# Kernel tuning notes

Hardware: AMD Instinct MI355X
Metric: run time of the kernel (lower is better)

The kernel has to match this reference:

```python
import jax, jax.numpy as jnp
import numpy as np

N_NODES = 100000

def gcn_layer(x, W, b, src, dst, norm):
    # x: [N, Fin], W: [Fin, Fout]; fused linear then normalized neighbor aggregation
    h = x @ W                                   # [N, Fout]
    msg = h[src] * norm[:, None]                # gather + per-edge scale, [E', Fout]
    agg = jax.ops.segment_sum(msg, dst, num_segments=N_NODES)  # scatter-add
    return agg + b

def _add_self_loops_and_norm(edge_index):
    src, dst = edge_index[0], edge_index[1]
    loop = jnp.arange(N_NODES, dtype=src.dtype)
    src = jnp.concatenate([src, loop])
    dst = jnp.concatenate([dst, loop])
    deg = jax.ops.segment_sum(jnp.ones_like(dst, dtype=jnp.float32), dst, num_segments=N_NODES)
    dis = jnp.where(deg > 0, jax.lax.rsqrt(deg), 0.0)   # deg^{-1/2}
    norm = dis[src] * dis[dst]                          # symmetric GCN normalization
    return src, dst, norm

def setup_inputs() -> dict:
    key = jax.random.key(0)
    k1, k2, k3, k4, k5, k6 = jax.random.split(key, 6)
    F_IN, F_HID, F_OUT = 64, 64, 64
    E = 1600000
    x = jax.random.normal(k1, (N_NODES, F_IN), dtype=jnp.float32)
    edge_index = jax.random.randint(k2, (2, E), 0, N_NODES, dtype=jnp.int64)
    s1 = 1.0 / np.sqrt(F_IN)
    s2 = 1.0 / np.sqrt(F_HID)
    W1 = jax.random.uniform(k3, (F_IN, F_HID), dtype=jnp.float32, minval=-s1, maxval=s1)
    b1 = jax.random.uniform(k4, (F_HID,), dtype=jnp.float32, minval=-s1, maxval=s1)
    W2 = jax.random.uniform(k5, (F_HID, F_OUT), dtype=jnp.float32, minval=-s2, maxval=s2)
    b2 = jax.random.uniform(k6, (F_OUT,), dtype=jnp.float32, minval=-s2, maxval=s2)
    return {"x": x, "edge_index": edge_index, "W1": W1, "b1": b1, "W2": W2, "b2": b2}

def reference(x, edge_index, W1, b1, W2, b2):
    src, dst, norm = _add_self_loops_and_norm(edge_index)
    h = gcn_layer(x, W1, b1, src, dst, norm)
    h = jax.nn.relu(h)
    h = gcn_layer(h, W2, b2, src, dst, norm)
    return h
```

## Files before the change

kernel.cpp:

```cpp
#include <hip/hip_runtime.h>
#include <cstdint>
#include <cstddef>


#define BK_SHIFT 9
#define BK_NODES 512
#define EPB 8192
#define CAP 12288
#define NBMAX 256

typedef short bf16x8 __attribute__((ext_vector_type(8)));
typedef float f32x4  __attribute__((ext_vector_type(4)));

static __device__ __forceinline__ unsigned short f2b(float f) {
    unsigned x = __float_as_uint(f);
    unsigned r = (x + 0x7FFFu + ((x >> 16) & 1u)) >> 16;
    return (unsigned short)r;
}
static __device__ __forceinline__ float blo(unsigned u) {
    return __uint_as_float(u << 16);
}
static __device__ __forceinline__ float bhi(unsigned u) {
    return __uint_as_float(u & 0xFFFF0000u);
}
static __device__ __forceinline__ void splitbf(float x, short& hi, short& lo) {
    unsigned short h = f2b(x);
    hi = (short)h;
    float r = x - __uint_as_float((unsigned)h << 16);
    lo = (short)f2b(r);
}

__global__ void k_init(int* __restrict__ gcursor, int NB) {
    int t = threadIdx.x;
    if (t < NB) gcursor[t] = t * CAP;
}

__global__ void __launch_bounds__(256) k_bscatter(const int* __restrict__ src,
                                                  const int* __restrict__ dst,
                                                  int* __restrict__ gcursor,
                                                  unsigned* __restrict__ packed,
                                                  int E, int NB) {
    __shared__ int hist[NBMAX];
    __shared__ int base[NBMAX];
    int t = threadIdx.x;
    for (int i = t; i < NB; i += 256) hist[i] = 0;
    __syncthreads();
    int e0 = blockIdx.x * EPB;
    int e1 = min(e0 + EPB, E);
    int4 dv[8];
    int kd[8];
#pragma unroll
    for (int k = 0; k < 8; ++k) {
        int e = e0 + t * 4 + k * 1024;
        kd[k] = (e + 3 < e1) ? 1 : 0;
        if (kd[k]) dv[k] = *(const int4*)(dst + e);
    }
#pragma unroll
    for (int k = 0; k < 8; ++k) {
        if (kd[k]) {
            atomicAdd(&hist[dv[k].x >> BK_SHIFT], 1);
            atomicAdd(&hist[dv[k].y >> BK_SHIFT], 1);
            atomicAdd(&hist[dv[k].z >> BK_SHIFT], 1);
            atomicAdd(&hist[dv[k].w >> BK_SHIFT], 1);
        }
    }
    __syncthreads();
    for (int i = t; i < NB; i += 256) {
        int c = hist[i];
        base[i] = c ? atomicAdd(&gcursor[i], c) : 0;
        hist[i] = 0;
    }
    __syncthreads();
    int4 sv[8];
#pragma unroll
    for (int k = 0; k < 8; ++k) {
        int e = e0 + t * 4 + k * 1024;
        if (kd[k]) sv[k] = *(const int4*)(src + e);
    }
#pragma unroll
    for (int k = 0; k < 8; ++k) {
        if (kd[k]) {
            int b0 = dv[k].x >> BK_SHIFT;
            int p0 = base[b0] + atomicAdd(&hist[b0], 1);
            packed[p0] = (unsigned)sv[k].x | (((unsigned)dv[k].x & (BK_NODES - 1)) << 17);
            int b1 = dv[k].y >> BK_SHIFT;
            int p1 = base[b1] + atomicAdd(&hist[b1], 1);
            packed[p1] = (unsigned)sv[k].y | (((unsigned)dv[k].y & (BK_NODES - 1)) << 17);
            int b2 = dv[k].z >> BK_SHIFT;
            int p2 = base[b2] + atomicAdd(&hist[b2], 1);
            packed[p2] = (unsigned)sv[k].z | (((unsigned)dv[k].z & (BK_NODES - 1)) << 17);
            int b3 = dv[k].w >> BK_SHIFT;
            int p3 = base[b3] + atomicAdd(&hist[b3], 1);
            packed[p3] = (unsigned)sv[k].w | (((unsigned)dv[k].w & (BK_NODES - 1)) << 17);
        }
    }
}

__global__ void __launch_bounds__(512) k_build(const unsigned* __restrict__ packed,
                                               const int* __restrict__ gcursor,
                                               int* __restrict__ rp,
                                               int* __restrict__ dega,
                                               float* __restrict__ dis,
                                               int* __restrict__ col, int N) {
    __shared__ int cnt_s[BK_NODES];
    __shared__ int tmp[BK_NODES];
    int b = blockIdx.x;
    int t = threadIdx.x;
    int node0 = b << BK_SHIFT;
    int nnode = min(BK_NODES, N - node0);
    int e0 = b * CAP;
    int e1 = gcursor[b];
    cnt_s[t] = 0;
    __syncthreads();
    for (int e = e0 + t * 4; e < e1; e += 2048) {
        int m = e1 - e; m = m > 4 ? 4 : m;
        unsigned p0 = packed[e];
        unsigned p1 = (m > 1) ? packed[e + 1] : 0;
        unsigned p2 = (m > 2) ? packed[e + 2] : 0;
        unsigned p3 = (m > 3) ? packed[e + 3] : 0;
        atomicAdd(&cnt_s[p0 >> 17], 1);
        if (m > 1) atomicAdd(&cnt_s[p1 >> 17], 1);
        if (m > 2) atomicAdd(&cnt_s[p2 >> 17], 1);
        if (m > 3) atomicAdd(&cnt_s[p3 >> 17], 1);
    }
    __syncthreads();
    int v = cnt_s[t];
    tmp[t] = v;
    __syncthreads();
    for (int off = 1; off < BK_NODES; off <<= 1) {
        int a = (t >= off) ? tmp[t - off] : 0;
        __syncthreads();
        tmp[t] += a;
        __syncthreads();
    }
    int excl = tmp[t] - v;
    if (t < nnode) {
        rp[node0 + t] = e0 + excl;
        dega[node0 + t] = v;
        dis[node0 + t] = rsqrtf((float)(v + 1));
    }
    __syncthreads();
    cnt_s[t] = excl;
    __syncthreads();
    for (int e = e0 + t * 4; e < e1; e += 2048) {
        int m = e1 - e; m = m > 4 ? 4 : m;
        unsigned p0 = packed[e];
        unsigned p1 = (m > 1) ? packed[e + 1] : 0;
        unsigned p2 = (m > 2) ? packed[e + 2] : 0;
        unsigned p3 = (m > 3) ? packed[e + 3] : 0;
        int pos0 = atomicAdd(&cnt_s[p0 >> 17], 1);
        col[e0 + pos0] = (int)(p0 & 0x1FFFFu);
        if (m > 1) { int pos = atomicAdd(&cnt_s[p1 >> 17], 1); col[e0 + pos] = (int)(p1 & 0x1FFFFu); }
        if (m > 2) { int pos = atomicAdd(&cnt_s[p2 >> 17], 1); col[e0 + pos] = (int)(p2 & 0x1FFFFu); }
        if (m > 3) { int pos = atomicAdd(&cnt_s[p3 >> 17], 1); col[e0 + pos] = (int)(p3 & 0x1FFFFu); }
    }
}

__global__ void __launch_bounds__(256) k_gemm_mfma(const float* __restrict__ X,
                                                   const float* __restrict__ W,
                                                   const float* __restrict__ dis,
                                                   unsigned short* __restrict__ g16,
                                                   int n, int nstrips) {
    __shared__ float Ws[4096];
    int t = threadIdx.x;
    {
        const float4* W4 = (const float4*)W;
        float4* S4 = (float4*)Ws;
#pragma unroll
        for (int i = 0; i < 4; ++i) S4[t + i * 256] = W4[t + i * 256];
    }
    __syncthreads();
    int wid  = t >> 6;
    int lane = t & 63;
    int quad = lane >> 4;
    int fl   = lane & 15;

    bf16x8 Bh[4][2], Bl[4][2];
#pragma unroll
    for (int tt = 0; tt < 4; ++tt)
#pragma unroll
        for (int c = 0; c < 2; ++c)
#pragma unroll
            for (int j = 0; j < 8; ++j) {
                float w = Ws[(c * 32 + quad * 8 + j) * 64 + tt * 16 + fl];
                short hi, lo;
                splitbf(w, hi, lo);
                Bh[tt][c][j] = hi;
                Bl[tt][c][j] = lo;
            }

    for (int s = blockIdx.x * 4 + wid; s < nstrips; s += gridDim.x * 4) {
        int row0 = s << 4;
        const float4* xp = (const float4*)(X + ((size_t)(row0 + fl) << 6));
        bf16x8 Ah[2], Al[2];
#pragma unroll
        for (int c = 0; c < 2; ++c) {
            float4 a = xp[c * 8 + quad * 2];
            float4 b = xp[c * 8 + quad * 2 + 1];
            float xs[8] = {a.x, a.y, a.z, a.w, b.x, b.y, b.z, b.w};
#pragma unroll
            for (int j = 0; j < 8; ++j) {
                short hi, lo;
                splitbf(xs[j], hi, lo);
                Ah[c][j] = hi;
                Al[c][j] = lo;
            }
        }
        f32x4 acc[4];
#pragma unroll
        for (int tt = 0; tt < 4; ++tt) acc[tt] = (f32x4){0.f, 0.f, 0.f, 0.f};
#pragma unroll
        for (int tt = 0; tt < 4; ++tt) {
#pragma unroll
            for (int c = 0; c < 2; ++c) {
                acc[tt] = __builtin_amdgcn_mfma_f32_16x16x32_bf16(Ah[c], Bh[tt][c], acc[tt], 0, 0, 0);
                acc[tt] = __builtin_amdgcn_mfma_f32_16x16x32_bf16(Al[c], Bh[tt][c], acc[tt], 0, 0, 0);
                acc[tt] = __builtin_amdgcn_mfma_f32_16x16x32_bf16(Ah[c], Bl[tt][c], acc[tt], 0, 0, 0);
            }
        }
        float4 dv = *(const float4*)(dis + row0 + quad * 4);
        float ds4[4] = {dv.x, dv.y, dv.z, dv.w};
#pragma unroll
        for (int tt = 0; tt < 4; ++tt) {
#pragma unroll
            for (int r = 0; r < 4; ++r) {
                int row = row0 + quad * 4 + r;
                float v = acc[tt][r] * ds4[r];
                g16[(size_t)row * 64 + tt * 16 + fl] = f2b(v);
            }
        }
    }
}

template <int RELU>
__global__ void __launch_bounds__(256) k_agg(const unsigned short* __restrict__ g16,
                                             const int* __restrict__ col,
                                             const int* __restrict__ rp,
                                             const int* __restrict__ dega,
                                             const float* __restrict__ dis,
                                             const float* __restrict__ bias,
                                             float* __restrict__ out, int n) {
    int lane = threadIdx.x & 63;
    int wv = (blockIdx.x << 2) | (threadIdx.x >> 6);
    int sub = lane >> 3;
    int fl  = lane & 7;
    int base = wv << 3;
    if (base >= n) return;
    int node = base + sub;
    int nd = min(node, n - 1);
    int start = rp[nd];
    int deg = (node < n) ? dega[nd] : 0;
    int dm = max(deg, __shfl_xor(deg, 8));
    dm = max(dm, __shfl_xor(dm, 16));
    dm = max(dm, __shfl_xor(dm, 32));

    uint4 us = *((const uint4*)(g16 + ((size_t)nd << 6)) + fl);
    float A[8], B[8], C[8], D[8];
    A[0] = blo(us.x); A[1] = bhi(us.x); A[2] = blo(us.y); A[3] = bhi(us.y);
    A[4] = blo(us.z); A[5] = bhi(us.z); A[6] = blo(us.w); A[7] = bhi(us.w);
#pragma unroll
    for (int j = 0; j < 8; ++j) { B[j] = 0.f; C[j] = 0.f; D[j] = 0.f; }

    int sb = sub << 3;
    for (int c = 0; c < dm; c += 8) {
        int rem = deg - c;
        int cv = 0;
        if (fl < rem) cv = col[start + c + fl];
        int rr[8];
#pragma unroll
        for (int i = 0; i < 8; ++i) rr[i] = __shfl(cv, sb + i);
        uint4 u[8];
#pragma unroll
        for (int i = 0; i < 8; ++i)
            if (i < rem) u[i] = *((const uint4*)(g16 + ((size_t)rr[i] << 6)) + fl);
#pragma unroll
        for (int i = 0; i < 8; ++i) {
            if (i < rem) {
                float* T = ((i & 3) == 0) ? A : ((i & 3) == 1) ? B : ((i & 3) == 2) ? C : D;
                T[0] += blo(u[i].x); T[1] += bhi(u[i].x);
                T[2] += blo(u[i].y); T[3] += bhi(u[i].y);
                T[4] += blo(u[i].z); T[5] += bhi(u[i].z);
                T[6] += blo(u[i].w); T[7] += bhi(u[i].w);
            }
        }
    }
    float s = dis[nd];
    float4 bv0 = ((const float4*)bias)[fl * 2];
    float4 bv1 = ((const float4*)bias)[fl * 2 + 1];
    float r[8];
#pragma unroll
    for (int j = 0; j < 8; ++j) r[j] = (A[j] + B[j]) + (C[j] + D[j]);
    float4 o0, o1;
    o0.x = fmaf(s, r[0], bv0.x); o0.y = fmaf(s, r[1], bv0.y);
    o0.z = fmaf(s, r[2], bv0.z); o0.w = fmaf(s, r[3], bv0.w);
    o1.x = fmaf(s, r[4], bv1.x); o1.y = fmaf(s, r[5], bv1.y);
    o1.z = fmaf(s, r[6], bv1.z); o1.w = fmaf(s, r[7], bv1.w);
    if (RELU) {
        o0.x = fmaxf(o0.x, 0.f); o0.y = fmaxf(o0.y, 0.f);
        o0.z = fmaxf(o0.z, 0.f); o0.w = fmaxf(o0.w, 0.f);
        o1.x = fmaxf(o1.x, 0.f); o1.y = fmaxf(o1.y, 0.f);
        o1.z = fmaxf(o1.z, 0.f); o1.w = fmaxf(o1.w, 0.f);
    }
    if (node < n) {
        float4* op = (float4*)(out + ((size_t)node << 6)) + fl * 2;
        op[0] = o0;
        op[1] = o1;
    }
}

__global__ void __launch_bounds__(256, 4) k_agg_gemm2(const unsigned short* __restrict__ g16,
                                                      const int* __restrict__ col,
                                                      const int* __restrict__ rp,
                                                      const int* __restrict__ dega,
                                                      const float* __restrict__ dis,
                                                      const float* __restrict__ bias,
                                                      const float* __restrict__ W2,
                                                      unsigned short* __restrict__ g16b,
                                                      int n) {
    __shared__ float W2s[4096];
    __shared__ float hs[32 * 68];
    int t = threadIdx.x;
    {
        const float4* W4 = (const float4*)W2;
        float4* S4 = (float4*)W2s;
#pragma unroll
        for (int i = 0; i < 4; ++i) S4[t + i * 256] = W4[t + i * 256];
    }

    int lane = t & 63;
    int wid  = t >> 6;
    int wv = (blockIdx.x << 2) | wid;
    int sub = lane >> 3;
    int fl  = lane & 7;
    int base = wv << 3;
    int node = base + sub;
    int nd = (node < n) ? node : (n - 1);
    int start = rp[nd];
    int deg = (node < n) ? dega[nd] : 0;
    int dm = max(deg, __shfl_xor(deg, 8));
    dm = max(dm, __shfl_xor(dm, 16));
    dm = max(dm, __shfl_xor(dm, 32));

    uint4 us = *((const uint4*)(g16 + ((size_t)nd << 6)) + fl);
    float A[8], B[8], C[8], D[8];
    A[0] = blo(us.x); A[1] = bhi(us.x); A[2] = blo(us.y); A[3] = bhi(us.y);
    A[4] = blo(us.z); A[5] = bhi(us.z); A[6] = blo(us.w); A[7] = bhi(us.w);
#pragma unroll
    for (int j = 0; j < 8; ++j) { B[j] = 0.f; C[j] = 0.f; D[j] = 0.f; }

    int sb = sub << 3;
    for (int c = 0; c < dm; c += 8) {
        int rem = deg - c;
        int cv = 0;
        if (fl < rem) cv = col[start + c + fl];
        int rr[8];
#pragma unroll
        for (int i = 0; i < 8; ++i) rr[i] = __shfl(cv, sb + i);
        uint4 u[8];
#pragma unroll
        for (int i = 0; i < 8; ++i)
            if (i < rem) u[i] = *((const uint4*)(g16 + ((size_t)rr[i] << 6)) + fl);
#pragma unroll
        for (int i = 0; i < 8; ++i) {
            if (i < rem) {
                float* T = ((i & 3) == 0) ? A : ((i & 3) == 1) ? B : ((i & 3) == 2) ? C : D;
                T[0] += blo(u[i].x); T[1] += bhi(u[i].x);
                T[2] += blo(u[i].y); T[3] += bhi(u[i].y);
                T[4] += blo(u[i].z); T[5] += bhi(u[i].z);
                T[6] += blo(u[i].w); T[7] += bhi(u[i].w);
            }
        }
    }
    {
        float s = dis[nd];
        float4 bv0 = ((const float4*)bias)[fl * 2];
        float4 bv1 = ((const float4*)bias)[fl * 2 + 1];
        float r[8];
#pragma unroll
        for (int j = 0; j < 8; ++j) r[j] = (A[j] + B[j]) + (C[j] + D[j]);
        float4 h0, h1;
        h0.x = fmaxf(fmaf(s, r[0], bv0.x), 0.f);
        h0.y = fmaxf(fmaf(s, r[1], bv0.y), 0.f);
        h0.z = fmaxf(fmaf(s, r[2], bv0.z), 0.f);
        h0.w = fmaxf(fmaf(s, r[3], bv0.w), 0.f);
        h1.x = fmaxf(fmaf(s, r[4], bv1.x), 0.f);
        h1.y = fmaxf(fmaf(s, r[5], bv1.y), 0.f);
        h1.z = fmaxf(fmaf(s, r[6], bv1.z), 0.f);
        h1.w = fmaxf(fmaf(s, r[7], bv1.w), 0.f);
        int lrow = (wid << 3) | sub;
        float* hp = &hs[lrow * 68 + fl * 8];
        *(float4*)hp = h0;
        *(float4*)(hp + 4) = h1;
    }
    __syncthreads();

    {
        int quad = lane >> 4;
        int fq   = lane & 15;
        int strip = wid >> 1;
        int tbase = (wid & 1) << 1;
        bf16x8 Ah[2], Al[2];
#pragma unroll
        for (int kc = 0; kc < 2; ++kc) {
            const float* hp2 = &hs[(strip * 16 + fq) * 68 + kc * 32 + quad * 8];
            float4 a = *(const float4*)hp2;
            float4 b = *(const float4*)(hp2 + 4);
            float xs[8] = {a.x, a.y, a.z, a.w, b.x, b.y, b.z, b.w};
#pragma unroll
            for (int j = 0; j < 8; ++j) {
                short hi, lo;
                splitbf(xs[j], hi, lo);
                Ah[kc][j] = hi;
                Al[kc][j] = lo;
            }
        }
        f32x4 acc[2];
        acc[0] = (f32x4){0.f, 0.f, 0.f, 0.f};
        acc[1] = (f32x4){0.f, 0.f, 0.f, 0.f};
#pragma unroll
        for (int tt = 0; tt < 2; ++tt) {
#pragma unroll
            for (int kc = 0; kc < 2; ++kc) {
                bf16x8 Bh, Bl;
#pragma unroll
                for (int j = 0; j < 8; ++j) {
                    float w = W2s[(kc * 32 + quad * 8 + j) * 64 + (tbase + tt) * 16 + fq];
                    short hi, lo;
                    splitbf(w, hi, lo);
                    Bh[j] = hi;
                    Bl[j] = lo;
                }
                acc[tt] = __builtin_amdgcn_mfma_f32_16x16x32_bf16(Ah[kc], Bh, acc[tt], 0, 0, 0);
                acc[tt] = __builtin_amdgcn_mfma_f32_16x16x32_bf16(Al[kc], Bh, acc[tt], 0, 0, 0);
                acc[tt] = __builtin_amdgcn_mfma_f32_16x16x32_bf16(Ah[kc], Bl, acc[tt], 0, 0, 0);
            }
        }
        int row0 = (blockIdx.x << 5) + strip * 16 + quad * 4;
        float d4[4];
        if (row0 + 3 < n) {
            float4 dv = *(const float4*)(dis + row0);
            d4[0] = dv.x; d4[1] = dv.y; d4[2] = dv.z; d4[3] = dv.w;
        } else {
#pragma unroll
            for (int r2 = 0; r2 < 4; ++r2) d4[r2] = (row0 + r2 < n) ? dis[row0 + r2] : 0.f;
        }
#pragma unroll
        for (int tt = 0; tt < 2; ++tt) {
#pragma unroll
            for (int r2 = 0; r2 < 4; ++r2) {
                int row = row0 + r2;
                if (row < n)
                    g16b[(size_t)row * 64 + (tbase + tt) * 16 + fq] = f2b(acc[tt][r2] * d4[r2]);
            }
        }
    }
}

extern "C" void kernel_launch(void* const* d_in, const int* in_sizes, int n_in,
                              void* d_out, int out_size, void* d_ws, size_t ws_size,
                              hipStream_t stream) {
    const float* x  = (const float*)d_in[0];
    const int*   ei = (const int*)d_in[1];
    const float* W1 = (const float*)d_in[2];
    const float* b1 = (const float*)d_in[3];
    const float* W2 = (const float*)d_in[4];
    const float* b2 = (const float*)d_in[5];
    float* out = (float*)d_out;

    const int N = in_sizes[0] / 64;
    const int E = in_sizes[1] / 2;
    const int NB = (N + BK_NODES - 1) >> BK_SHIFT;
    const int nstrips = (N + 15) >> 4;
    const int* src = ei;
    const int* dst = ei + E;

    char* ws = (char*)d_ws;
    size_t off = 0;
    auto alloc = [&](size_t bytes) -> void* {
        void* p = ws + off;
        off = (off + bytes + 255) & ~(size_t)255;
        return p;
    };
    int*            gcursor = (int*)alloc((size_t)NB * 4);
    int*            rp      = (int*)alloc((size_t)N * 4);
    int*            dega    = (int*)alloc((size_t)N * 4);
    float*          dis     = (float*)alloc((size_t)N * 4);
    unsigned*       packed  = (unsigned*)alloc((size_t)NB * CAP * 4);
    int*            col     = (int*)alloc((size_t)NB * CAP * 4);
    unsigned short* g16     = (unsigned short*)alloc((size_t)N * 64 * 2);
    unsigned short* g16b    = (unsigned short*)alloc((size_t)N * 64 * 2);
    (void)ws_size;

    k_init<<<1, 256, 0, stream>>>(gcursor, NB);
    k_bscatter<<<(E + EPB - 1) / EPB, 256, 0, stream>>>(src, dst, gcursor, packed, E, NB);
    k_build<<<NB, 512, 0, stream>>>(packed, gcursor, rp, dega, dis, col, N);

    k_gemm_mfma<<<782, 256, 0, stream>>>(x, W1, dis, g16, N, nstrips);
    k_agg_gemm2<<<(N + 31) / 32, 256, 0, stream>>>(g16, col, rp, dega, dis, b1, W2, g16b, N);
    k_agg<0><<<(N + 31) / 32, 256, 0, stream>>>(g16b, col, rp, dega, dis, b2, out, N);
}
```

Baseline: 199.3 us.

## Shrink CSR buckets, stage packed edges in LDS, and pad W2 shared tile

Node buckets shrink from 512 to 256 nodes, with smaller per-block edge chunks and capacity, so there are twice as many buckets and build blocks, each using 256 threads. The build kernel now copies each bucket's packed edges into shared memory once with vector loads, then runs both counting passes from LDS instead of reading global memory twice. The W2 shared tile in the second aggregation kernel gets a row stride of 66 to reduce LDS bank conflicts on the strided B-operand reads. The tighter per-bucket capacity of 5120 adds overflow risk if a bucket receives more edges than expected.

```diff
diff --git a/kernel.cpp b/kernel.cpp
--- a/kernel.cpp
+++ b/kernel.cpp
@@ -3,11 +3,11 @@
 #include <cstddef>
 
 
-#define BK_SHIFT 9
-#define BK_NODES 512
-#define EPB 8192
-#define CAP 12288
-#define NBMAX 256
+#define BK_SHIFT 8
+#define BK_NODES 256
+#define EPB 4096
+#define CAP 5120
+#define NBMAX 512
 
 typedef short bf16x8 __attribute__((ext_vector_type(8)));
 typedef float f32x4  __attribute__((ext_vector_type(4)));
@@ -47,16 +47,16 @@
     __syncthreads();
     int e0 = blockIdx.x * EPB;
     int e1 = min(e0 + EPB, E);
-    int4 dv[8];
-    int kd[8];
-#pragma unroll
-    for (int k = 0; k < 8; ++k) {
+    int4 dv[4];
+    int kd[4];
+#pragma unroll
+    for (int k = 0; k < 4; ++k) {
         int e = e0 + t * 4 + k * 1024;
         kd[k] = (e + 3 < e1) ? 1 : 0;
         if (kd[k]) dv[k] = *(const int4*)(dst + e);
     }
 #pragma unroll
-    for (int k = 0; k < 8; ++k) {
+    for (int k = 0; k < 4; ++k) {
         if (kd[k]) {
             atomicAdd(&hist[dv[k].x >> BK_SHIFT], 1);
             atomicAdd(&hist[dv[k].y >> BK_SHIFT], 1);
@@ -71,14 +71,14 @@
         hist[i] = 0;
     }
     __syncthreads();
-    int4 sv[8];
-#pragma unroll
-    for (int k = 0; k < 8; ++k) {
+    int4 sv[4];
+#pragma unroll
+    for (int k = 0; k < 4; ++k) {
         int e = e0 + t * 4 + k * 1024;
         if (kd[k]) sv[k] = *(const int4*)(src + e);
     }
 #pragma unroll
-    for (int k = 0; k < 8; ++k) {
+    for (int k = 0; k < 4; ++k) {
         if (kd[k]) {
             int b0 = dv[k].x >> BK_SHIFT;
             int p0 = base[b0] + atomicAdd(&hist[b0], 1);
@@ -96,12 +96,13 @@
     }
 }
 
-__global__ void __launch_bounds__(512) k_build(const unsigned* __restrict__ packed,
+__global__ void __launch_bounds__(256) k_build(const unsigned* __restrict__ packed,
                                                const int* __restrict__ gcursor,
                                                int* __restrict__ rp,
                                                int* __restrict__ dega,
                                                float* __restrict__ dis,
                                                int* __restrict__ col, int N) {
+    __shared__ unsigned pk_s[CAP];
     __shared__ int cnt_s[BK_NODES];
     __shared__ int tmp[BK_NODES];
     int b = blockIdx.x;
@@ -109,20 +110,18 @@
     int node0 = b << BK_SHIFT;
     int nnode = min(BK_NODES, N - node0);
     int e0 = b * CAP;
-    int e1 = gcursor[b];
+    int count = gcursor[b] - e0;
     cnt_s[t] = 0;
-    __syncthreads();
-    for (int e = e0 + t * 4; e < e1; e += 2048) {
-        int m = e1 - e; m = m > 4 ? 4 : m;
-        unsigned p0 = packed[e];
-        unsigned p1 = (m > 1) ? packed[e + 1] : 0;
-        unsigned p2 = (m > 2) ? packed[e + 2] : 0;
-        unsigned p3 = (m > 3) ? packed[e + 3] : 0;
-        atomicAdd(&cnt_s[p0 >> 17], 1);
-        if (m > 1) atomicAdd(&cnt_s[p1 >> 17], 1);
-        if (m > 2) atomicAdd(&cnt_s[p2 >> 17], 1);
-        if (m > 3) atomicAdd(&cnt_s[p3 >> 17], 1);
-    }
+    for (int e4 = t * 4; e4 < count; e4 += 1024) {
+        if (e4 + 3 < count) {
+            uint4 v = *(const uint4*)(packed + e0 + e4);
+            *(uint4*)&pk_s[e4] = v;
+        } else {
+            for (int m = e4; m < count; ++m) pk_s[m] = packed[e0 + m];
+        }
+    }
+    __syncthreads();
+    for (int j = t; j < count; j += 256) atomicAdd(&cnt_s[pk_s[j] >> 17], 1);
     __syncthreads();
     int v = cnt_s[t];
     tmp[t] = v;
@@ -142,17 +141,10 @@
     __syncthreads();
     cnt_s[t] = excl;
     __syncthreads();
-    for (int e = e0 + t * 4; e < e1; e += 2048) {
-        int m = e1 - e; m = m > 4 ? 4 : m;
-        unsigned p0 = packed[e];
-        unsigned p1 = (m > 1) ? packed[e + 1] : 0;
-        unsigned p2 = (m > 2) ? packed[e + 2] : 0;
-        unsigned p3 = (m > 3) ? packed[e + 3] : 0;
-        int pos0 = atomicAdd(&cnt_s[p0 >> 17], 1);
-        col[e0 + pos0] = (int)(p0 & 0x1FFFFu);
-        if (m > 1) { int pos = atomicAdd(&cnt_s[p1 >> 17], 1); col[e0 + pos] = (int)(p1 & 0x1FFFFu); }
-        if (m > 2) { int pos = atomicAdd(&cnt_s[p2 >> 17], 1); col[e0 + pos] = (int)(p2 & 0x1FFFFu); }
-        if (m > 3) { int pos = atomicAdd(&cnt_s[p3 >> 17], 1); col[e0 + pos] = (int)(p3 & 0x1FFFFu); }
+    for (int j = t; j < count; j += 256) {
+        unsigned p = pk_s[j];
+        int pos = atomicAdd(&cnt_s[p >> 17], 1);
+        col[e0 + pos] = (int)(p & 0x1FFFFu);
     }
 }
 
@@ -317,14 +309,18 @@
                                                       const float* __restrict__ W2,
                                                       unsigned short* __restrict__ g16b,
                                                       int n) {
-    __shared__ float W2s[4096];
+    __shared__ float W2s[64 * 66];
     __shared__ float hs[32 * 68];
     int t = threadIdx.x;
     {
         const float4* W4 = (const float4*)W2;
-        float4* S4 = (float4*)W2s;
-#pragma unroll
-        for (int i = 0; i < 4; ++i) S4[t + i * 256] = W4[t + i * 256];
+#pragma unroll
+        for (int i = 0; i < 4; ++i) {
+            float4 v = W4[t + i * 256];
+            int idx = (t + i * 256) << 2;
+            float* p = &W2s[(idx >> 6) * 66 + (idx & 63)];
+            p[0] = v.x; p[1] = v.y; p[2] = v.z; p[3] = v.w;
+        }
     }
 
     int lane = t & 63;
@@ -424,7 +420,7 @@
                 bf16x8 Bh, Bl;
 #pragma unroll
                 for (int j = 0; j < 8; ++j) {
-                    float w = W2s[(kc * 32 + quad * 8 + j) * 64 + (tbase + tt) * 16 + fq];
+                    float w = W2s[(kc * 32 + quad * 8 + j) * 66 + (tbase + tt) * 16 + fq];
                     short hi, lo;
                     splitbf(w, hi, lo);
                     Bh[j] = hi;
@@ -491,9 +487,9 @@
     unsigned short* g16b    = (unsigned short*)alloc((size_t)N * 64 * 2);
     (void)ws_size;
 
-    k_init<<<1, 256, 0, stream>>>(gcursor, NB);
+    k_init<<<1, 512, 0, stream>>>(gcursor, NB);
     k_bscatter<<<(E + EPB - 1) / EPB, 256, 0, stream>>>(src, dst, gcursor, packed, E, NB);
-    k_build<<<NB, 512, 0, stream>>>(packed, gcursor, rp, dega, dis, col, N);
+    k_build<<<NB, 256, 0, stream>>>(packed, gcursor, rp, dega, dis, col, N);
 
     k_gemm_mfma<<<782, 256, 0, stream>>>(x, W1, dis, g16, N, nstrips);
     k_agg_gemm2<<<(N + 31) / 32, 256, 0, stream>>>(g16, col, rp, dega, dis, b1, W2, g16b, N);
```

Measured after the change: 200.8 us. No clear change (+0.8%).

## Split neighbor aggregation into four feature passes with 4-byte gathers

Applied to the files above, without the earlier changes.

Both aggregation kernels now loop over four 16-feature slices of each row. Each lane gathers one 4-byte word per neighbor per pass instead of a 16-byte vector, which cuts accumulator registers from 32 to 8 floats. Column indices are read with nontemporal loads, and the final output is written with nontemporal stores. The cost is that the edge list is reread and shuffled four times, and the gathers become narrower, so more memory transactions are issued per byte.

```diff
diff --git a/kernel.cpp b/kernel.cpp
--- a/kernel.cpp
+++ b/kernel.cpp
@@ -11,6 +11,7 @@
 
 typedef short bf16x8 __attribute__((ext_vector_type(8)));
 typedef float f32x4  __attribute__((ext_vector_type(4)));
+typedef float f32x2  __attribute__((ext_vector_type(2)));
 
 static __device__ __forceinline__ unsigned short f2b(float f) {
     unsigned x = __float_as_uint(f);
@@ -232,7 +233,6 @@
     }
 }
 
-template <int RELU>
 __global__ void __launch_bounds__(256) k_agg(const unsigned short* __restrict__ g16,
                                              const int* __restrict__ col,
                                              const int* __restrict__ rp,
@@ -253,58 +253,44 @@
     int dm = max(deg, __shfl_xor(deg, 8));
     dm = max(dm, __shfl_xor(dm, 16));
     dm = max(dm, __shfl_xor(dm, 32));
-
-    uint4 us = *((const uint4*)(g16 + ((size_t)nd << 6)) + fl);
-    float A[8], B[8], C[8], D[8];
-    A[0] = blo(us.x); A[1] = bhi(us.x); A[2] = blo(us.y); A[3] = bhi(us.y);
-    A[4] = blo(us.z); A[5] = bhi(us.z); A[6] = blo(us.w); A[7] = bhi(us.w);
-#pragma unroll
-    for (int j = 0; j < 8; ++j) { B[j] = 0.f; C[j] = 0.f; D[j] = 0.f; }
-
+    float s = dis[nd];
+    const unsigned* g16u = (const unsigned*)g16;
     int sb = sub << 3;
-    for (int c = 0; c < dm; c += 8) {
-        int rem = deg - c;
-        int cv = 0;
-        if (fl < rem) cv = col[start + c + fl];
-        int rr[8];
-#pragma unroll
-        for (int i = 0; i < 8; ++i) rr[i] = __shfl(cv, sb + i);
-        uint4 u[8];
-#pragma unroll
-        for (int i = 0; i < 8; ++i)
-            if (i < rem) u[i] = *((const uint4*)(g16 + ((size_t)rr[i] << 6)) + fl);
-#pragma unroll
-        for (int i = 0; i < 8; ++i) {
-            if (i < rem) {
-                float* T = ((i & 3) == 0) ? A : ((i & 3) == 1) ? B : ((i & 3) == 2) ? C : D;
-                T[0] += blo(u[i].x); T[1] += bhi(u[i].x);
-                T[2] += blo(u[i].y); T[3] += bhi(u[i].y);
-                T[4] += blo(u[i].z); T[5] += bhi(u[i].z);
-                T[6] += blo(u[i].w); T[7] += bhi(u[i].w);
-            }
-        }
-    }
-    float s = dis[nd];
-    float4 bv0 = ((const float4*)bias)[fl * 2];
-    float4 bv1 = ((const float4*)bias)[fl * 2 + 1];
-    float r[8];
-#pragma unroll
-    for (int j = 0; j < 8; ++j) r[j] = (A[j] + B[j]) + (C[j] + D[j]);
-    float4 o0, o1;
-    o0.x = fmaf(s, r[0], bv0.x); o0.y = fmaf(s, r[1], bv0.y);
-    o0.z = fmaf(s, r[2], bv0.z); o0.w = fmaf(s, r[3], bv0.w);
-    o1.x = fmaf(s, r[4], bv1.x); o1.y = fmaf(s, r[5], bv1.y);
-    o1.z = fmaf(s, r[6], bv1.z); o1.w = fmaf(s, r[7], bv1.w);
-    if (RELU) {
-        o0.x = fmaxf(o0.x, 0.f); o0.y = fmaxf(o0.y, 0.f);
-        o0.z = fmaxf(o0.z, 0.f); o0.w = fmaxf(o0.w, 0.f);
-        o1.x = fmaxf(o1.x, 0.f); o1.y = fmaxf(o1.y, 0.f);
-        o1.z = fmaxf(o1.z, 0.f); o1.w = fmaxf(o1.w, 0.f);
-    }
-    if (node < n) {
-        float4* op = (float4*)(out + ((size_t)node << 6)) + fl * 2;
-        op[0] = o0;
-        op[1] = o1;
+
+#pragma unroll 1
+    for (int p = 0; p < 4; ++p) {
+        unsigned us = g16u[(size_t)nd * 32 + p * 8 + fl];
+        float A0 = blo(us), A1 = bhi(us);
+        float B0 = 0.f, B1 = 0.f, C0 = 0.f, C1 = 0.f, D0 = 0.f, D1 = 0.f;
+        for (int c = 0; c < dm; c += 8) {
+            int rem = deg - c;
+            int cv = 0;
+            if (fl < rem) cv = __builtin_nontemporal_load(col + start + c + fl);
+            int rr[8];
+#pragma unroll
+            for (int i = 0; i < 8; ++i) rr[i] = __shfl(cv, sb + i);
+            unsigned u[8];
+#pragma unroll
+            for (int i = 0; i < 8; ++i)
+                if (i < rem) u[i] = g16u[(size_t)rr[i] * 32 + p * 8 + fl];
+#pragma unroll
+            for (int i = 0; i < 8; ++i) {
+                if (i < rem) {
+                    if ((i & 3) == 0)      { A0 += blo(u[i]); A1 += bhi(u[i]); }
+                    else if ((i & 3) == 1) { B0 += blo(u[i]); B1 += bhi(u[i]); }
+                    else if ((i & 3) == 2) { C0 += blo(u[i]); C1 += bhi(u[i]); }
+                    else                   { D0 += blo(u[i]); D1 += bhi(u[i]); }
+                }
+            }
+        }
+        float r0 = (A0 + B0) + (C0 + D0);
+        float r1 = (A1 + B1) + (C1 + D1);
+        f32x2 bv = *(const f32x2*)(bias + p * 16 + fl * 2);
+        f32x2 o;
+        o[0] = fmaf(s, r0, bv[0]);
+        o[1] = fmaf(s, r1, bv[1]);
+        if (node < n)
+            __builtin_nontemporal_store(o, (f32x2*)(out + ((size_t)node << 6) + p * 16 + fl * 2));
     }
 }
 
@@ -340,57 +326,49 @@
     int dm = max(deg, __shfl_xor(deg, 8));
     dm = max(dm, __shfl_xor(dm, 16));
     dm = max(dm, __shfl_xor(dm, 32));
-
-    uint4 us = *((const uint4*)(g16 + ((size_t)nd << 6)) + fl);
-    float A[8], B[8], C[8], D[8];
-    A[0] = blo(us.x); A[1] = bhi(us.x); A[2] = blo(us.y); A[3] = bhi(us.y);
-    A[4] = blo(us.z); A[5] = bhi(us.z); A[6] = blo(us.w); A[7] = bhi(us.w);
-#pragma unroll
-    for (int j = 0; j < 8; ++j) { B[j] = 0.f; C[j] = 0.f; D[j] = 0.f; }
-
+    float s = dis[nd];
+    const unsigned* g16u = (const unsigned*)g16;
     int sb = sub << 3;
-    for (int c = 0; c < dm; c += 8) {
-        int rem = deg - c;
-        int cv = 0;
-        if (fl < rem) cv = col[start + c + fl];
-        int rr[8];
-#pragma unroll
-        for (int i = 0; i < 8; ++i) rr[i] = __shfl(cv, sb + i);
-        uint4 u[8];
-#pragma unroll
-        for (int i = 0; i < 8; ++i)
-            if (i < rem) u[i] = *((const uint4*)(g16 + ((size_t)rr[i] << 6)) + fl);
-#pragma unroll
-        for (int i = 0; i < 8; ++i) {
-            if (i < rem) {
-                float* T = ((i & 3) == 0) ? A : ((i & 3) == 1) ? B : ((i & 3) == 2) ? C : D;
-                T[0] += blo(u[i].x); T[1] += bhi(u[i].x);
-                T[2] += blo(u[i].y); T[3] += bhi(u[i].y);
-                T[4] += blo(u[i].z); T[5] += bhi(u[i].z);
-                T[6] += blo(u[i].w); T[7] += bhi(u[i].w);
-            }
-        }
-    }
-    {
-        float s = dis[nd];
-        float4 bv0 = ((const float4*)bias)[fl * 2];
-        float4 bv1 = ((const float4*)bias)[fl * 2 + 1];
-        float r[8];
-#pragma unroll
-        for (int j = 0; j < 8; ++j) r[j] = (A[j] + B[j]) + (C[j] + D[j]);
-        float4 h0, h1;
-        h0.x = fmaxf(fmaf(s, r[0], bv0.x), 0.f);
-        h0.y = fmaxf(fmaf(s, r[1], bv0.y), 0.f);
-        h0.z = fmaxf(fmaf(s, r[2], bv0.z), 0.f);
-        h0.w = fmaxf(fmaf(s, r[3], bv0.w), 0.f);
-        h1.x = fmaxf(fmaf(s, r[4], bv1.x), 0.f);
-        h1.y = fmaxf(fmaf(s, r[5], bv1.y), 0.f);
-        h1.z = fmaxf(fmaf(s, r[6], bv1.z), 0.f);
-        h1.w = fmaxf(fmaf(s, r[7], bv1.w), 0.f);
-        int lrow = (wid << 3) | sub;
-        float* hp = &hs[lrow * 68 + fl * 8];
-        *(float4*)hp = h0;
-        *(float4*)(hp + 4) = h1;
+    int lrow = (wid << 3) | sub;
+
+#pragma unroll 1
+    for (int p = 0; p < 4; ++p) {
+        unsigned us = g16u[(size_t)nd * 32 + p * 8 + fl];
+        float A0 = blo(us), A1 = bhi(us);
+        float B0 = 0.f, B1 = 0.f, C0 = 0.f, C1 = 0.f, D0 = 0.f, D1 = 0.f;
+        for (int c = 0; c < dm; c += 8) {
+            int rem = deg - c;
+            int cv = 0;
+            if (fl < rem) cv = __builtin_nontemporal_load(col + start + c + fl);
+            int rr[8];
+#pragma unroll
+            for (int i = 0; i < 8; ++i) rr[i] = __shfl(cv, sb + i);
+            unsigned u[8];
+#pragma unroll
+            for (int i = 0; i < 8; ++i)
+                if (i < rem) u[i] = g16u[(size_t)rr[i] * 32 + p * 8 + fl];
+#pragma unroll
+            for (int i = 0; i < 8; ++i) {
+                if (i < rem) {
+                    if ((i & 3) == 0)      { A0 += blo(u[i]); A1 += bhi(u[i]); }
+                    else if ((i & 3) == 1) { B0 += blo(u[i]); B1 += bhi(u[i]); }
+                    else if ((i & 3) == 2) { C0 += blo(u[i]); C1 += bhi(u[i]); }
+                    else                   { D0 += blo(u[i]); D1 += bhi(u[i]); }
+                }
+            }
+        }
+        float r0 = (A0 + B0) + (C0 + D0);
+        float r1 = (A1 + B1) + (C1 + D1);
+        f32x2 bv = *(const f32x2*)(bias + p * 16 + fl * 2);
+        f32x2 h2;
+        if (node < n) {
+            h2[0] = fmaxf(fmaf(s, r0, bv[0]), 0.f);
+            h2[1] = fmaxf(fmaf(s, r1, bv[1]), 0.f);
+        } else {
+            h2[0] = 0.f;
+            h2[1] = 0.f;
+        }
+        *(f32x2*)&hs[lrow * 68 + p * 16 + fl * 2] = h2;
     }
     __syncthreads();
 
@@ -497,5 +475,5 @@
 
     k_gemm_mfma<<<782, 256, 0, stream>>>(x, W1, dis, g16, N, nstrips);
     k_agg_gemm2<<<(N + 31) / 32, 256, 0, stream>>>(g16, col, rp, dega, dis, b1, W2, g16b, N);
-    k_agg<0><<<(N + 31) / 32, 256, 0, stream>>>(g16b, col, rp, dega, dis, b2, out, N);
-}
+    k_agg<<<(N + 31) / 32, 256, 0, stream>>>(g16b, col, rp, dega, dis, b2, out, N);
+}
```

Measured after the change: 335.4 us. 68.3% more time.
